# Kernel tuning notes

Measured on AMD Instinct MI355X. Metric: run time of the kernel, lower is better.

Reference implementation:

```python
import jax, jax.numpy as jnp
import numpy as np
from jax import lax

REPR, ACT, HID = 256, 2, 512
BN_EPS = 1e-5


def setup_inputs() -> dict:
    key = jax.random.key(0)
    ks = jax.random.split(key, 12)
    B, H, W, Tm1 = 512, 64, 64, 16
    d_in = REPR + ACT
    s = lambda k, shape, scale: jax.random.normal(k, shape, dtype=jnp.float32) * scale
    return {
        "init_state": jax.random.normal(ks[0], (B, 2, H, W), dtype=jnp.float32),
        "actions": jax.random.normal(ks[1], (B, Tm1, ACT), dtype=jnp.float32),
        "conv_w": s(ks[2], (16, 2, 3, 3), (1.0 / np.sqrt(2 * 9))),
        "bn_gamma": jnp.ones((16,), jnp.float32),
        "bn_beta": jnp.zeros((16,), jnp.float32),
        "enc_fc_w": s(ks[3], (REPR, 16), (1.0 / np.sqrt(16))),
        "enc_fc_b": s(ks[4], (REPR,), 0.01),
        "gru_w_ih": s(ks[5], (3 * HID, d_in), (1.0 / np.sqrt(HID))),
        "gru_w_hh": s(ks[6], (3 * HID, HID), (1.0 / np.sqrt(HID))),
        "gru_b_ih": s(ks[7], (3 * HID,), (1.0 / np.sqrt(HID))),
        "gru_b_hh": s(ks[8], (3 * HID,), (1.0 / np.sqrt(HID))),
        "pred_fc_w": s(ks[9], (REPR, HID), (1.0 / np.sqrt(HID))),
        "pred_fc_b": s(ks[10], (REPR,), 0.01),
    }


def _encoder(x, conv_w, bn_gamma, bn_beta, enc_fc_w, enc_fc_b):
    # Conv2d(2->16, 3x3, stride 1, pad 1, no bias), NCHW
    y = lax.conv_general_dilated(x, conv_w, (1, 1), "SAME",
                                 dimension_numbers=("NCHW", "OIHW", "NCHW"))
    # BatchNorm2d in training mode: batch statistics over (N, H, W)
    mean = jnp.mean(y, axis=(0, 2, 3), keepdims=True)
    var = jnp.var(y, axis=(0, 2, 3), keepdims=True)
    y = (y - mean) * lax.rsqrt(var + BN_EPS)
    y = y * bn_gamma[None, :, None, None] + bn_beta[None, :, None, None]
    y = jax.nn.relu(y)
    # MaxPool2d(2, 2)
    y = lax.reduce_window(y, -jnp.inf, lax.max, (1, 1, 2, 2), (1, 1, 2, 2), "VALID")
    # AdaptiveAvgPool2d((1,1)) + flatten
    y = jnp.mean(y, axis=(2, 3))  # (B, 16)
    return y @ enc_fc_w.T + enc_fc_b  # (B, repr_dim)


def reference(init_state, actions, conv_w, bn_gamma, bn_beta, enc_fc_w, enc_fc_b,
              gru_w_ih, gru_w_hh, gru_b_ih, gru_b_hh, pred_fc_w, pred_fc_b):
    B = init_state.shape[0]
    s0 = _encoder(init_state, conv_w, bn_gamma, bn_beta, enc_fc_w, enc_fc_b)  # (B, R)

    def step(carry, u_t):
        s_prev, h = carry
        x = jnp.concatenate([s_prev, u_t], axis=-1)          # (B, R+A)
        gx = x @ gru_w_ih.T + gru_b_ih                        # (B, 3H)
        gh = h @ gru_w_hh.T + gru_b_hh                        # (B, 3H)
        gx_r, gx_z, gx_n = jnp.split(gx, 3, axis=-1)
        gh_r, gh_z, gh_n = jnp.split(gh, 3, axis=-1)
        r = jax.nn.sigmoid(gx_r + gh_r)
        z = jax.nn.sigmoid(gx_z + gh_z)
        n = jnp.tanh(gx_n + r * gh_n)
        h_new = (1.0 - z) * n + z * h
        s_pred = jax.nn.relu(h_new @ pred_fc_w.T + pred_fc_b)  # (B, R)
        return (s_pred, h_new), s_pred

    h0 = jnp.zeros((B, HID), dtype=s0.dtype)
    u_seq = jnp.transpose(actions, (1, 0, 2))  # (T-1, B, A)
    _, preds = lax.scan(step, (s0, h0), u_seq)  # preds: (T-1, B, R)
    pred_encs = jnp.concatenate([s0[None], preds], axis=0)  # (T, B, R)
    return jnp.transpose(pred_encs, (1, 0, 2))  # (B, T, R)
```

## Files before the change

### kernel.cpp

```cpp
#include <hip/hip_runtime.h>
#include <hip/hip_bf16.h>
#include <math.h>

#define TM1 16
#define TT 17

typedef __attribute__((ext_vector_type(8))) __bf16 bf16x8;
typedef __attribute__((ext_vector_type(4))) float f32x4;

#define OFF_BSTATS 0
#define OFF_STATS  65536
#define OFF_POOLED 65568
#define OFF_BCOL   98336
#define OFF_SPB    104480
#define OFF_PWB    170016
#define OFF_WIHB   235552
#define OFF_WHHB   432160
#define OFF_HB     825376

#define IMG_STRIDE 67
#define SLAB_ROWS 18
#define IMG_CI (SLAB_ROWS * IMG_STRIDE)

__device__ __forceinline__ void stage_slab(float* __restrict__ imgp,
                                           const float* __restrict__ xb, int slab, int tid) {
  for (int i = tid; i < 2 * SLAB_ROWS * 66; i += 256) {
    const int ci = i / (SLAB_ROWS * 66);
    const int rem = i - ci * (SLAB_ROWS * 66);
    const int lr = rem / 66, c = rem - lr * 66;
    const int gr = slab * 16 - 1 + lr;
    float v = 0.0f;
    if (gr >= 0 && gr < 64 && c >= 1 && c <= 64) v = xb[ci * 4096 + gr * 64 + (c - 1)];
    imgp[ci * IMG_CI + lr * IMG_STRIDE + c] = v;
  }
}

__global__ __launch_bounds__(256) void enc_stats_prep(
    const float* __restrict__ x, const float* __restrict__ cw,
    float* __restrict__ bstats,
    const float* __restrict__ wih, const float* __restrict__ whh,
    const float* __restrict__ pw,
    const float* __restrict__ bih, const float* __restrict__ bhh,
    __hip_bfloat16* __restrict__ wihb, __hip_bfloat16* __restrict__ whhb,
    __hip_bfloat16* __restrict__ pwb, float* __restrict__ bcol) {
  {
    const int n1 = 1536 * 256, n2 = 1536 * 512, n3 = 256 * 512, n4 = 512 * 12;
    int i = blockIdx.x * 256 + threadIdx.x;
    int st = gridDim.x * 256;
    for (int j = i; j < n1 + n2 + n3 + n4; j += st) {
      if (j < n1) {
        int r = j >> 8, c = j & 255;
        wihb[j] = __float2bfloat16(wih[r * 258 + c]);
      } else if (j < n1 + n2) {
        int k = j - n1;
        whhb[k] = __float2bfloat16(whh[k]);
      } else if (j < n1 + n2 + n3) {
        int k = j - n1 - n2;
        pwb[k] = __float2bfloat16(pw[k]);
      } else {
        int k = j - n1 - n2 - n3;
        int col = k / 12, e = k - col * 12;
        float v = 0.0f;
        switch (e) {
          case 0: v = bih[col] + bhh[col]; break;
          case 1: v = bih[512 + col] + bhh[512 + col]; break;
          case 2: v = bih[1024 + col]; break;
          case 3: v = bhh[1024 + col]; break;
          case 4: v = wih[col * 258 + 256]; break;
          case 5: v = wih[col * 258 + 257]; break;
          case 6: v = wih[(512 + col) * 258 + 256]; break;
          case 7: v = wih[(512 + col) * 258 + 257]; break;
          case 8: v = wih[(1024 + col) * 258 + 256]; break;
          case 9: v = wih[(1024 + col) * 258 + 257]; break;
          default: v = 0.0f; break;
        }
        bcol[k] = v;
      }
    }
  }

  __shared__ float imgp[2 * IMG_CI];
  __shared__ float reds[4][16], redq[4][16];
  const int tid = threadIdx.x;
  const int b = blockIdx.x >> 2, slab = blockIdx.x & 3;
  const int wv = tid >> 6;
  stage_slab(imgp, x + b * 8192, slab, tid);
  __syncthreads();

  const int pr = tid >> 5;
  const int pc = tid & 31;

  float rv[2][4][4];
#pragma unroll
  for (int ci = 0; ci < 2; ++ci)
#pragma unroll
    for (int dy = 0; dy < 4; ++dy)
#pragma unroll
      for (int j = 0; j < 4; ++j)
        rv[ci][dy][j] = imgp[ci * IMG_CI + (2 * pr + dy) * IMG_STRIDE + 2 * pc + j];

  float s[16], q[16];
#pragma unroll
  for (int c = 0; c < 16; ++c) { s[c] = 0.0f; q[c] = 0.0f; }

#pragma unroll
  for (int c4 = 0; c4 < 4; ++c4) {
    float a[4][4];
#pragma unroll
    for (int ch = 0; ch < 4; ++ch)
#pragma unroll
      for (int p = 0; p < 4; ++p) a[ch][p] = 0.0f;
#pragma unroll
    for (int ci = 0; ci < 2; ++ci) {
      float wk[4][9];
#pragma unroll
      for (int ch = 0; ch < 4; ++ch)
#pragma unroll
        for (int k = 0; k < 9; ++k)
          wk[ch][k] = cw[(c4 * 4 + ch) * 18 + ci * 9 + k];
#pragma unroll
      for (int ry = 0; ry < 2; ++ry)
#pragma unroll
        for (int rx = 0; rx < 2; ++rx)
#pragma unroll
          for (int ch = 0; ch < 4; ++ch) {
            float acc = a[ch][ry * 2 + rx];
#pragma unroll
            for (int dy = 0; dy < 3; ++dy) {
              acc = fmaf(wk[ch][dy * 3 + 0], rv[ci][ry + dy][rx + 0], acc);
              acc = fmaf(wk[ch][dy * 3 + 1], rv[ci][ry + dy][rx + 1], acc);
              acc = fmaf(wk[ch][dy * 3 + 2], rv[ci][ry + dy][rx + 2], acc);
            }
            a[ch][ry * 2 + rx] = acc;
          }
    }
#pragma unroll
    for (int ch = 0; ch < 4; ++ch)
#pragma unroll
      for (int p = 0; p < 4; ++p) {
        const float v = a[ch][p];
        s[c4 * 4 + ch] += v;
        q[c4 * 4 + ch] = fmaf(v, v, q[c4 * 4 + ch]);
      }
  }

#pragma unroll
  for (int c = 0; c < 16; ++c) {
    float sv = s[c], qv = q[c];
#pragma unroll
    for (int off = 32; off >= 1; off >>= 1) {
      sv += __shfl_down(sv, off);
      qv += __shfl_down(qv, off);
    }
    if ((tid & 63) == 0) { reds[wv][c] = sv; redq[wv][c] = qv; }
  }
  __syncthreads();
  if (tid < 16)
    bstats[tid * 2048 + blockIdx.x] =
        reds[0][tid] + reds[1][tid] + reds[2][tid] + reds[3][tid];
  else if (tid < 32) {
    int c = tid - 16;
    bstats[tid * 2048 + blockIdx.x] =
        redq[0][c] + redq[1][c] + redq[2][c] + redq[3][c];
  }
}

__global__ __launch_bounds__(256) void reduce_stats_k(const float* __restrict__ bstats,
                                                      float* __restrict__ stats) {
  __shared__ float acc[4];
  const int c = blockIdx.x, tid = threadIdx.x;
  const float4 v4 = *(const float4*)(bstats + c * 2048 + tid * 8);
  const float4 w4 = *(const float4*)(bstats + c * 2048 + tid * 8 + 4);
  float v = v4.x + v4.y + v4.z + v4.w + w4.x + w4.y + w4.z + w4.w;
#pragma unroll
  for (int off = 32; off >= 1; off >>= 1) v += __shfl_down(v, off);
  if ((tid & 63) == 0) acc[tid >> 6] = v;
  __syncthreads();
  if (tid == 0) stats[c] = acc[0] + acc[1] + acc[2] + acc[3];
}

__global__ __launch_bounds__(256) void enc_pool(const float* __restrict__ x,
                                                const float* __restrict__ cw,
                                                const float* __restrict__ stats,
                                                const float* __restrict__ gamma,
                                                const float* __restrict__ beta,
                                                float* __restrict__ pooledG) {
  __shared__ float imgp[2 * IMG_CI];
  __shared__ float red[4][16];
  __shared__ float statsL[32];
  const int tid = threadIdx.x;
  const int b = blockIdx.x >> 2, slab = blockIdx.x & 3;
  const int wv = tid >> 6;
  stage_slab(imgp, x + b * 8192, slab, tid);
  if (tid < 32) statsL[tid] = stats[tid];
  __syncthreads();

  const float invN = 1.0f / (512.0f * 4096.0f);
  const int pr = tid >> 5;
  const int pc = tid & 31;

  float rv[2][4][4];
#pragma unroll
  for (int ci = 0; ci < 2; ++ci)
#pragma unroll
    for (int dy = 0; dy < 4; ++dy)
#pragma unroll
      for (int j = 0; j < 4; ++j)
        rv[ci][dy][j] = imgp[ci * IMG_CI + (2 * pr + dy) * IMG_STRIDE + 2 * pc + j];

  float psum[16];
#pragma unroll
  for (int c = 0; c < 16; ++c) psum[c] = 0.0f;

#pragma unroll
  for (int c4 = 0; c4 < 4; ++c4) {
    float a[4][4];
#pragma unroll
    for (int ch = 0; ch < 4; ++ch)
#pragma unroll
      for (int p = 0; p < 4; ++p) a[ch][p] = 0.0f;
#pragma unroll
    for (int ci = 0; ci < 2; ++ci) {
      float wk[4][9];
#pragma unroll
      for (int ch = 0; ch < 4; ++ch)
#pragma unroll
        for (int k = 0; k < 9; ++k)
          wk[ch][k] = cw[(c4 * 4 + ch) * 18 + ci * 9 + k];
#pragma unroll
      for (int ry = 0; ry < 2; ++ry)
#pragma unroll
        for (int rx = 0; rx < 2; ++rx)
#pragma unroll
          for (int ch = 0; ch < 4; ++ch) {
            float acc = a[ch][ry * 2 + rx];
#pragma unroll
            for (int dy = 0; dy < 3; ++dy) {
              acc = fmaf(wk[ch][dy * 3 + 0], rv[ci][ry + dy][rx + 0], acc);
              acc = fmaf(wk[ch][dy * 3 + 1], rv[ci][ry + dy][rx + 1], acc);
              acc = fmaf(wk[ch][dy * 3 + 2], rv[ci][ry + dy][rx + 2], acc);
            }
            a[ch][ry * 2 + rx] = acc;
          }
    }
#pragma unroll
    for (int ch = 0; ch < 4; ++ch) {
      const int c = c4 * 4 + ch;
      const float m = statsL[c] * invN;
      const float var = statsL[16 + c] * invN - m * m;
      const float isd = rsqrtf(var + 1e-5f);
      const float sc = gamma[c] * isd;
      const float sh = beta[c] - m * sc;
      const float v0 = fmaxf(fmaf(a[ch][0], sc, sh), 0.0f);
      const float v1 = fmaxf(fmaf(a[ch][1], sc, sh), 0.0f);
      const float v2 = fmaxf(fmaf(a[ch][2], sc, sh), 0.0f);
      const float v3 = fmaxf(fmaf(a[ch][3], sc, sh), 0.0f);
      psum[c] += fmaxf(fmaxf(v0, v1), fmaxf(v2, v3));
    }
  }

#pragma unroll
  for (int c = 0; c < 16; ++c) {
    float v = psum[c];
#pragma unroll
    for (int off = 32; off >= 1; off >>= 1) v += __shfl_down(v, off);
    if ((tid & 63) == 0) red[wv][c] = v;
  }
  __syncthreads();
  if (tid < 16)
    pooledG[blockIdx.x * 16 + tid] = red[0][tid] + red[1][tid] + red[2][tid] + red[3][tid];
}

__global__ __launch_bounds__(384) void gru_v2(
    const __hip_bfloat16* __restrict__ spb,
    const __hip_bfloat16* __restrict__ hb_in,
    __hip_bfloat16* __restrict__ hb_out,
    const __hip_bfloat16* __restrict__ wihb,
    const __hip_bfloat16* __restrict__ whhb,
    const float* __restrict__ bcol,
    const float* __restrict__ actions,
    const float* __restrict__ pooledG,
    const float* __restrict__ fcw,
    const float* __restrict__ fcb,
    float* __restrict__ out,
    int t) {
  __shared__ __hip_bfloat16 sF[8 * 64 * 8];
  __shared__ __hip_bfloat16 hF[16 * 64 * 8];
  __shared__ float accL[4][2][256];
  const int tid = threadIdx.x;
  const int w = tid / 64, lane = tid & 63;
  const int l15 = lane & 15, hi = lane >> 4;
  const int cg = blockIdx.x, band = blockIdx.y;
  const int row0 = band * 16;
  const int ct = w & 1, g = w >> 1;

  if (t == 0) {
    float* avgF = &accL[0][0][0];
    if (tid < 256) {
      const int r = tid >> 4, k = tid & 15;
      const int img = row0 + r;
      const float v = pooledG[(img * 4 + 0) * 16 + k] + pooledG[(img * 4 + 1) * 16 + k] +
                      pooledG[(img * 4 + 2) * 16 + k] + pooledG[(img * 4 + 3) * 16 + k];
      avgF[r * 16 + k] = v * (1.0f / 1024.0f);
    }
    __syncthreads();
    for (int i = tid; i < 4096; i += 384) {
      const int kk = i >> 9, rem = i & 511, ln = rem >> 3, e = rem & 7;
      const int r = ln & 15;
      const int col = kk * 32 + (ln >> 4) * 8 + e;
      float v = fcb[col];
#pragma unroll
      for (int k = 0; k < 16; ++k) v = fmaf(avgF[r * 16 + k], fcw[col * 16 + k], v);
      sF[i] = __float2bfloat16(v);
      if (cg == 0) out[((size_t)(row0 + r) * TT + 0) * 256 + col] = v;
    }
  } else {
    for (int i = tid; i < 512; i += 384) {
      int kk = i >> 6, ln = i & 63;
      *(bf16x8*)(sF + i * 8) =
          *(const bf16x8*)(spb + (row0 + (ln & 15)) * 256 + kk * 32 + (ln >> 4) * 8);
    }
    for (int i = tid; i < 1024; i += 384) {
      int kk = i >> 6, ln = i & 63;
      *(bf16x8*)(hF + i * 8) =
          *(const bf16x8*)(hb_in + (row0 + (ln & 15)) * 512 + kk * 32 + (ln >> 4) * 8);
    }
  }
  __syncthreads();

  const int cj = cg * 32 + ct * 16;
  f32x4 accS = {0.f, 0.f, 0.f, 0.f}, accH = accS;
  {
    const __hip_bfloat16* B = wihb + (g * 512 + cj + l15) * 256 + hi * 8;
#pragma unroll
    for (int kk = 0; kk < 8; ++kk) {
      bf16x8 a = *(const bf16x8*)(sF + (kk * 64 + lane) * 8);
      accS = __builtin_amdgcn_mfma_f32_16x16x32_bf16(a, *(const bf16x8*)(B + kk * 32),
                                                     accS, 0, 0, 0);
    }
  }
  if (t > 0) {
    const __hip_bfloat16* B = whhb + (g * 512 + cj + l15) * 512 + hi * 8;
#pragma unroll
    for (int kk = 0; kk < 16; ++kk) {
      bf16x8 a = *(const bf16x8*)(hF + (kk * 64 + lane) * 8);
      accH = __builtin_amdgcn_mfma_f32_16x16x32_bf16(a, *(const bf16x8*)(B + kk * 32),
                                                     accH, 0, 0, 0);
    }
  }
  __syncthreads();
  if (g < 2) {
#pragma unroll
    for (int i = 0; i < 4; ++i)
      accL[g][ct][(hi * 4 + i) * 16 + l15] = accS[i] + accH[i];
  } else {
#pragma unroll
    for (int i = 0; i < 4; ++i) {
      accL[2][ct][(hi * 4 + i) * 16 + l15] = accS[i];
      accL[3][ct][(hi * 4 + i) * 16 + l15] = accH[i];
    }
  }
  __syncthreads();

  if (w < 2) {
    f32x4 vR = *(const f32x4*)&accL[0][w][lane * 4];
    f32x4 vZ = *(const f32x4*)&accL[1][w][lane * 4];
    f32x4 vXN = *(const f32x4*)&accL[2][w][lane * 4];
    f32x4 vHN = *(const f32x4*)&accL[3][w][lane * 4];
    const int r = lane >> 2;
    const int row = row0 + r;
    const float u0 = actions[row * 32 + t * 2 + 0];
    const float u1 = actions[row * 32 + t * 2 + 1];
#pragma unroll
    for (int j = 0; j < 4; ++j) {
      const int c = (lane & 3) * 4 + j;
      const int col = cg * 32 + w * 16 + c;
      const float4 b0 = *(const float4*)(bcol + col * 12);
      const float4 b1 = *(const float4*)(bcol + col * 12 + 4);
      const float4 b2 = *(const float4*)(bcol + col * 12 + 8);
      const float gr = vR[j] + b0.x + u0 * b1.x + u1 * b1.y;
      const float gz = vZ[j] + b0.y + u0 * b1.z + u1 * b1.w;
      const float gxn = vXN[j] + b0.z + u0 * b2.x + u1 * b2.y;
      const float ghn = vHN[j] + b0.w;
      const float rg = 1.0f / (1.0f + __expf(-gr));
      const float zg = 1.0f / (1.0f + __expf(-gz));
      float xn = gxn + rg * ghn;
      xn = fminf(fmaxf(xn, -15.0f), 15.0f);
      const float e = __expf(2.0f * xn);
      const float ng = (e - 1.0f) / (e + 1.0f);
      const float hp = (t > 0) ? (float)hb_in[row * 512 + col] : 0.0f;
      const float hnv = (1.0f - zg) * ng + zg * hp;
      hb_out[row * 512 + col] = __float2bfloat16(hnv);
    }
  }
}

__global__ __launch_bounds__(256) void pred_v2(
    const __hip_bfloat16* __restrict__ hb,
    const __hip_bfloat16* __restrict__ pwb,
    const float* __restrict__ pb,
    float* __restrict__ out,
    __hip_bfloat16* __restrict__ spb,
    int slot) {
  __shared__ float accL[4][256];
  const int tid = threadIdx.x;
  const int w = tid >> 6, lane = tid & 63;
  const int l15 = lane & 15, hi = lane >> 4;
  const int pcg = blockIdx.x, band = blockIdx.y;
  const int row0 = band * 16, pc0 = pcg * 16;
  f32x4 acc = {0.f, 0.f, 0.f, 0.f};
  const __hip_bfloat16* A = hb + (row0 + l15) * 512 + w * 128 + hi * 8;
  const __hip_bfloat16* B = pwb + (pc0 + l15) * 512 + w * 128 + hi * 8;
#pragma unroll
  for (int kk = 0; kk < 4; ++kk)
    acc = __builtin_amdgcn_mfma_f32_16x16x32_bf16(*(const bf16x8*)(A + kk * 32),
                                                  *(const bf16x8*)(B + kk * 32),
                                                  acc, 0, 0, 0);
#pragma unroll
  for (int i = 0; i < 4; ++i) accL[w][(hi * 4 + i) * 16 + l15] = acc[i];
  __syncthreads();
  if (w == 0) {
    f32x4 p0 = *(const f32x4*)&accL[0][lane * 4];
    f32x4 p1 = *(const f32x4*)&accL[1][lane * 4];
    f32x4 p2 = *(const f32x4*)&accL[2][lane * 4];
    f32x4 p3 = *(const f32x4*)&accL[3][lane * 4];
    const int r = lane >> 2;
    const int row = row0 + r;
    float4 ov;
    float* po = &ov.x;
#pragma unroll
    for (int j = 0; j < 4; ++j) {
      const int c = (lane & 3) * 4 + j;
      const int col = pc0 + c;
      float v = p0[j] + p1[j] + p2[j] + p3[j] + pb[col];
      v = fmaxf(v, 0.0f);
      po[j] = v;
      spb[row * 256 + col] = __float2bfloat16(v);
    }
    *(float4*)(out + ((size_t)row * TT + slot) * 256 + pc0 + (lane & 3) * 4) = ov;
  }
}

extern "C" void kernel_launch(void* const* d_in, const int* in_sizes, int n_in,
                              void* d_out, int out_size, void* d_ws, size_t ws_size,
                              hipStream_t stream) {
  const float* x       = (const float*)d_in[0];
  const float* actions = (const float*)d_in[1];
  const float* cw      = (const float*)d_in[2];
  const float* gamma   = (const float*)d_in[3];
  const float* beta    = (const float*)d_in[4];
  const float* fcw     = (const float*)d_in[5];
  const float* fcb     = (const float*)d_in[6];
  const float* wih     = (const float*)d_in[7];
  const float* whh     = (const float*)d_in[8];
  const float* bih     = (const float*)d_in[9];
  const float* bhh     = (const float*)d_in[10];
  const float* pw      = (const float*)d_in[11];
  const float* pb      = (const float*)d_in[12];
  float* out = (float*)d_out;
  float* ws  = (float*)d_ws;

  float* bstats  = ws + OFF_BSTATS;
  float* stats   = ws + OFF_STATS;
  float* pooledG = ws + OFF_POOLED;
  float* bcol    = ws + OFF_BCOL;
  __hip_bfloat16* spb  = (__hip_bfloat16*)(ws + OFF_SPB);
  __hip_bfloat16* pwb  = (__hip_bfloat16*)(ws + OFF_PWB);
  __hip_bfloat16* wihb = (__hip_bfloat16*)(ws + OFF_WIHB);
  __hip_bfloat16* whhb = (__hip_bfloat16*)(ws + OFF_WHHB);
  __hip_bfloat16* hb0  = (__hip_bfloat16*)(ws + OFF_HB);
  __hip_bfloat16* hb1  = hb0 + 512 * 512;

  enc_stats_prep<<<dim3(2048), dim3(256), 0, stream>>>(x, cw, bstats, wih, whh, pw,
                                                       bih, bhh, wihb, whhb, pwb, bcol);
  reduce_stats_k<<<dim3(32), dim3(256), 0, stream>>>(bstats, stats);
  enc_pool<<<dim3(2048), dim3(256), 0, stream>>>(x, cw, stats, gamma, beta, pooledG);
  for (int t = 0; t < TM1; ++t) {
    __hip_bfloat16* hbi = (t & 1) ? hb1 : hb0;
    __hip_bfloat16* hbo = (t & 1) ? hb0 : hb1;
    gru_v2<<<dim3(16, 32), dim3(384), 0, stream>>>(spb, hbi, hbo, wihb, whhb,
                                                   bcol, actions, pooledG, fcw, fcb,
                                                   out, t);
    pred_v2<<<dim3(16, 32), dim3(256), 0, stream>>>(hbo, pwb, pb, out, spb, t + 1);
  }
}
```

Baseline: 344.7 us.

## Compute encoder conv with bf16 MFMA implicit GEMM instead of scalar FMAs

Both encoder conv kernels (stats pass and pool pass) now stage the input slab in shared memory as bf16. Each wave gathers im2col fragments of 18 taps padded to 32 and runs the 3x3 conv as 16x16x32 bf16 MFMAs, with output channels as the N dimension. BN statistics and the ReLU/maxpool/sum are then computed straight from the MFMA accumulators, which removes the heavy per-thread scalar FMA loops. The trade-off is lower conv precision, half of each MFMA doing zero work, and scalar LDS gathers to build the fragments.

```diff
diff --git a/kernel.cpp b/kernel.cpp
--- a/kernel.cpp
+++ b/kernel.cpp
@@ -22,8 +22,9 @@
 #define SLAB_ROWS 18
 #define IMG_CI (SLAB_ROWS * IMG_STRIDE)
 
-__device__ __forceinline__ void stage_slab(float* __restrict__ imgp,
-                                           const float* __restrict__ xb, int slab, int tid) {
+__device__ __forceinline__ void stage_slab_bf16(__hip_bfloat16* __restrict__ imgp,
+                                                const float* __restrict__ xb, int slab,
+                                                int tid) {
   for (int i = tid; i < 2 * SLAB_ROWS * 66; i += 256) {
     const int ci = i / (SLAB_ROWS * 66);
     const int rem = i - ci * (SLAB_ROWS * 66);
@@ -31,8 +32,46 @@
     const int gr = slab * 16 - 1 + lr;
     float v = 0.0f;
     if (gr >= 0 && gr < 64 && c >= 1 && c <= 64) v = xb[ci * 4096 + gr * 64 + (c - 1)];
-    imgp[ci * IMG_CI + lr * IMG_STRIDE + c] = v;
-  }
+    imgp[ci * IMG_CI + lr * IMG_STRIDE + c] = __float2bfloat16(v);
+  }
+}
+
+__device__ __forceinline__ void make_k_offsets(int hi, int* off, int* val) {
+#pragma unroll
+  for (int j = 0; j < 8; ++j) {
+    const int k = hi * 8 + j;
+    if (k < 18) {
+      const int ci = k / 9, r9 = k - ci * 9;
+      const int dy = r9 / 3, dx = r9 - dy * 3;
+      off[j] = ci * IMG_CI + dy * IMG_STRIDE + dx;
+      val[j] = 1;
+    } else {
+      off[j] = 0;
+      val[j] = 0;
+    }
+  }
+}
+
+__device__ __forceinline__ bf16x8 make_conv_bfrag(const float* __restrict__ cw,
+                                                  int l15, int hi) {
+  __hip_bfloat16 btmp[8];
+#pragma unroll
+  for (int j = 0; j < 8; ++j) {
+    const int k = hi * 8 + j;
+    btmp[j] = __float2bfloat16((k < 18) ? cw[l15 * 18 + k] : 0.0f);
+  }
+  return *(bf16x8*)btmp;
+}
+
+__device__ __forceinline__ bf16x8 make_conv_afrag(const __hip_bfloat16* __restrict__ imgp,
+                                                  int yloc, int x0, int l15,
+                                                  const int* off, const int* val) {
+  const int base = yloc * IMG_STRIDE + x0 + l15;
+  const __hip_bfloat16 z = __float2bfloat16(0.0f);
+  __hip_bfloat16 atmp[8];
+#pragma unroll
+  for (int j = 0; j < 8; ++j) atmp[j] = val[j] ? imgp[base + off[j]] : z;
+  return *(bf16x8*)atmp;
 }
 
 __global__ __launch_bounds__(256) void enc_stats_prep(
@@ -79,89 +118,47 @@
     }
   }
 
-  __shared__ float imgp[2 * IMG_CI];
-  __shared__ float reds[4][16], redq[4][16];
+  __shared__ __hip_bfloat16 imgp[2 * IMG_CI];
+  __shared__ float redS[4][16], redQ[4][16];
   const int tid = threadIdx.x;
   const int b = blockIdx.x >> 2, slab = blockIdx.x & 3;
-  const int wv = tid >> 6;
-  stage_slab(imgp, x + b * 8192, slab, tid);
-  __syncthreads();
-
-  const int pr = tid >> 5;
-  const int pc = tid & 31;
-
-  float rv[2][4][4];
-#pragma unroll
-  for (int ci = 0; ci < 2; ++ci)
-#pragma unroll
-    for (int dy = 0; dy < 4; ++dy)
-#pragma unroll
-      for (int j = 0; j < 4; ++j)
-        rv[ci][dy][j] = imgp[ci * IMG_CI + (2 * pr + dy) * IMG_STRIDE + 2 * pc + j];
-
-  float s[16], q[16];
-#pragma unroll
-  for (int c = 0; c < 16; ++c) { s[c] = 0.0f; q[c] = 0.0f; }
-
-#pragma unroll
-  for (int c4 = 0; c4 < 4; ++c4) {
-    float a[4][4];
-#pragma unroll
-    for (int ch = 0; ch < 4; ++ch)
-#pragma unroll
-      for (int p = 0; p < 4; ++p) a[ch][p] = 0.0f;
-#pragma unroll
-    for (int ci = 0; ci < 2; ++ci) {
-      float wk[4][9];
-#pragma unroll
-      for (int ch = 0; ch < 4; ++ch)
-#pragma unroll
-        for (int k = 0; k < 9; ++k)
-          wk[ch][k] = cw[(c4 * 4 + ch) * 18 + ci * 9 + k];
-#pragma unroll
-      for (int ry = 0; ry < 2; ++ry)
-#pragma unroll
-        for (int rx = 0; rx < 2; ++rx)
-#pragma unroll
-          for (int ch = 0; ch < 4; ++ch) {
-            float acc = a[ch][ry * 2 + rx];
-#pragma unroll
-            for (int dy = 0; dy < 3; ++dy) {
-              acc = fmaf(wk[ch][dy * 3 + 0], rv[ci][ry + dy][rx + 0], acc);
-              acc = fmaf(wk[ch][dy * 3 + 1], rv[ci][ry + dy][rx + 1], acc);
-              acc = fmaf(wk[ch][dy * 3 + 2], rv[ci][ry + dy][rx + 2], acc);
-            }
-            a[ch][ry * 2 + rx] = acc;
-          }
-    }
-#pragma unroll
-    for (int ch = 0; ch < 4; ++ch)
-#pragma unroll
-      for (int p = 0; p < 4; ++p) {
-        const float v = a[ch][p];
-        s[c4 * 4 + ch] += v;
-        q[c4 * 4 + ch] = fmaf(v, v, q[c4 * 4 + ch]);
-      }
-  }
-
-#pragma unroll
-  for (int c = 0; c < 16; ++c) {
-    float sv = s[c], qv = q[c];
-#pragma unroll
-    for (int off = 32; off >= 1; off >>= 1) {
-      sv += __shfl_down(sv, off);
-      qv += __shfl_down(qv, off);
-    }
-    if ((tid & 63) == 0) { reds[wv][c] = sv; redq[wv][c] = qv; }
-  }
+  const int wv = tid >> 6, lane = tid & 63;
+  const int l15 = lane & 15, hi = lane >> 4;
+  stage_slab_bf16(imgp, x + b * 8192, slab, tid);
+
+  int off[8], val[8];
+  make_k_offsets(hi, off, val);
+  const bf16x8 bfrag = make_conv_bfrag(cw, l15, hi);
+  __syncthreads();
+
+  float sacc = 0.0f, qacc = 0.0f;
+  const f32x4 zero4 = {0.f, 0.f, 0.f, 0.f};
+#pragma unroll
+  for (int tp = 0; tp < 8; ++tp) {
+    const int tpi = wv * 8 + tp;
+    const int y0 = (tpi >> 2) * 2, x0 = (tpi & 3) * 16;
+    bf16x8 a0 = make_conv_afrag(imgp, y0, x0, l15, off, val);
+    bf16x8 a1 = make_conv_afrag(imgp, y0 + 1, x0, l15, off, val);
+    f32x4 c0 = __builtin_amdgcn_mfma_f32_16x16x32_bf16(a0, bfrag, zero4, 0, 0, 0);
+    f32x4 c1 = __builtin_amdgcn_mfma_f32_16x16x32_bf16(a1, bfrag, zero4, 0, 0, 0);
+#pragma unroll
+    for (int i = 0; i < 4; ++i) {
+      sacc += c0[i] + c1[i];
+      qacc = fmaf(c0[i], c0[i], qacc);
+      qacc = fmaf(c1[i], c1[i], qacc);
+    }
+  }
+  sacc += __shfl_down(sacc, 16); sacc += __shfl_down(sacc, 32);
+  qacc += __shfl_down(qacc, 16); qacc += __shfl_down(qacc, 32);
+  if (lane < 16) { redS[wv][l15] = sacc; redQ[wv][l15] = qacc; }
   __syncthreads();
   if (tid < 16)
     bstats[tid * 2048 + blockIdx.x] =
-        reds[0][tid] + reds[1][tid] + reds[2][tid] + reds[3][tid];
+        redS[0][tid] + redS[1][tid] + redS[2][tid] + redS[3][tid];
   else if (tid < 32) {
     int c = tid - 16;
     bstats[tid * 2048 + blockIdx.x] =
-        redq[0][c] + redq[1][c] + redq[2][c] + redq[3][c];
+        redQ[0][c] + redQ[1][c] + redQ[2][c] + redQ[3][c];
   }
 }
 
@@ -185,87 +182,50 @@
                                                 const float* __restrict__ gamma,
                                                 const float* __restrict__ beta,
                                                 float* __restrict__ pooledG) {
-  __shared__ float imgp[2 * IMG_CI];
+  __shared__ __hip_bfloat16 imgp[2 * IMG_CI];
   __shared__ float red[4][16];
   __shared__ float statsL[32];
   const int tid = threadIdx.x;
   const int b = blockIdx.x >> 2, slab = blockIdx.x & 3;
-  const int wv = tid >> 6;
-  stage_slab(imgp, x + b * 8192, slab, tid);
+  const int wv = tid >> 6, lane = tid & 63;
+  const int l15 = lane & 15, hi = lane >> 4;
+  stage_slab_bf16(imgp, x + b * 8192, slab, tid);
   if (tid < 32) statsL[tid] = stats[tid];
+
+  int off[8], val[8];
+  make_k_offsets(hi, off, val);
+  const bf16x8 bfrag = make_conv_bfrag(cw, l15, hi);
   __syncthreads();
 
   const float invN = 1.0f / (512.0f * 4096.0f);
-  const int pr = tid >> 5;
-  const int pc = tid & 31;
-
-  float rv[2][4][4];
-#pragma unroll
-  for (int ci = 0; ci < 2; ++ci)
-#pragma unroll
-    for (int dy = 0; dy < 4; ++dy)
-#pragma unroll
-      for (int j = 0; j < 4; ++j)
-        rv[ci][dy][j] = imgp[ci * IMG_CI + (2 * pr + dy) * IMG_STRIDE + 2 * pc + j];
-
-  float psum[16];
-#pragma unroll
-  for (int c = 0; c < 16; ++c) psum[c] = 0.0f;
-
-#pragma unroll
-  for (int c4 = 0; c4 < 4; ++c4) {
-    float a[4][4];
-#pragma unroll
-    for (int ch = 0; ch < 4; ++ch)
-#pragma unroll
-      for (int p = 0; p < 4; ++p) a[ch][p] = 0.0f;
-#pragma unroll
-    for (int ci = 0; ci < 2; ++ci) {
-      float wk[4][9];
-#pragma unroll
-      for (int ch = 0; ch < 4; ++ch)
-#pragma unroll
-        for (int k = 0; k < 9; ++k)
-          wk[ch][k] = cw[(c4 * 4 + ch) * 18 + ci * 9 + k];
-#pragma unroll
-      for (int ry = 0; ry < 2; ++ry)
-#pragma unroll
-        for (int rx = 0; rx < 2; ++rx)
-#pragma unroll
-          for (int ch = 0; ch < 4; ++ch) {
-            float acc = a[ch][ry * 2 + rx];
-#pragma unroll
-            for (int dy = 0; dy < 3; ++dy) {
-              acc = fmaf(wk[ch][dy * 3 + 0], rv[ci][ry + dy][rx + 0], acc);
-              acc = fmaf(wk[ch][dy * 3 + 1], rv[ci][ry + dy][rx + 1], acc);
-              acc = fmaf(wk[ch][dy * 3 + 2], rv[ci][ry + dy][rx + 2], acc);
-            }
-            a[ch][ry * 2 + rx] = acc;
-          }
-    }
-#pragma unroll
-    for (int ch = 0; ch < 4; ++ch) {
-      const int c = c4 * 4 + ch;
-      const float m = statsL[c] * invN;
-      const float var = statsL[16 + c] * invN - m * m;
-      const float isd = rsqrtf(var + 1e-5f);
-      const float sc = gamma[c] * isd;
-      const float sh = beta[c] - m * sc;
-      const float v0 = fmaxf(fmaf(a[ch][0], sc, sh), 0.0f);
-      const float v1 = fmaxf(fmaf(a[ch][1], sc, sh), 0.0f);
-      const float v2 = fmaxf(fmaf(a[ch][2], sc, sh), 0.0f);
-      const float v3 = fmaxf(fmaf(a[ch][3], sc, sh), 0.0f);
-      psum[c] += fmaxf(fmaxf(v0, v1), fmaxf(v2, v3));
-    }
-  }
-
-#pragma unroll
-  for (int c = 0; c < 16; ++c) {
-    float v = psum[c];
-#pragma unroll
-    for (int off = 32; off >= 1; off >>= 1) v += __shfl_down(v, off);
-    if ((tid & 63) == 0) red[wv][c] = v;
-  }
+  const float m = statsL[l15] * invN;
+  const float var = statsL[16 + l15] * invN - m * m;
+  const float isd = rsqrtf(var + 1e-5f);
+  const float scv = gamma[l15] * isd;
+  const float shv = beta[l15] - m * scv;
+
+  float psum = 0.0f;
+  const f32x4 zero4 = {0.f, 0.f, 0.f, 0.f};
+#pragma unroll
+  for (int tp = 0; tp < 8; ++tp) {
+    const int tpi = wv * 8 + tp;
+    const int y0 = (tpi >> 2) * 2, x0 = (tpi & 3) * 16;
+    bf16x8 a0 = make_conv_afrag(imgp, y0, x0, l15, off, val);
+    bf16x8 a1 = make_conv_afrag(imgp, y0 + 1, x0, l15, off, val);
+    f32x4 c0 = __builtin_amdgcn_mfma_f32_16x16x32_bf16(a0, bfrag, zero4, 0, 0, 0);
+    f32x4 c1 = __builtin_amdgcn_mfma_f32_16x16x32_bf16(a1, bfrag, zero4, 0, 0, 0);
+#pragma unroll
+    for (int p = 0; p < 2; ++p) {
+      const float v00 = fmaxf(fmaf(c0[2 * p + 0], scv, shv), 0.0f);
+      const float v01 = fmaxf(fmaf(c0[2 * p + 1], scv, shv), 0.0f);
+      const float v10 = fmaxf(fmaf(c1[2 * p + 0], scv, shv), 0.0f);
+      const float v11 = fmaxf(fmaf(c1[2 * p + 1], scv, shv), 0.0f);
+      psum += fmaxf(fmaxf(v00, v01), fmaxf(v10, v11));
+    }
+  }
+  psum += __shfl_down(psum, 16);
+  psum += __shfl_down(psum, 32);
+  if (lane < 16) red[wv][l15] = psum;
   __syncthreads();
   if (tid < 16)
     pooledG[blockIdx.x * 16 + tid] = red[0][tid] + red[1][tid] + red[2][tid] + red[3][tid];
```

New measurement: 335.6 us. -2.6%, faster.
